# Kernel optimization log

Measured on AMD Instinct MI355X. Metric: run time of the kernel, lower is better.

Reference implementation:

```python
import jax, jax.numpy as jnp
import numpy as np

H = 16          # num_heads
K = 15          # kernel_size (padding_l = K-1, causal)
EPS = 1e-5      # LayerNorm eps


def setup_inputs() -> dict:
    key = jax.random.key(0)
    ks = jax.random.split(key, 8)
    T, B, C, F = 1024, 8, 1024, 4096
    n = lambda k, shape, scale=1.0: jax.random.normal(k, shape, jnp.float32) * scale
    return {
        "x": n(ks[0], (T, B, C)),
        "w_lin": n(ks[1], (C, H * K), 0.02),      # dynamic-conv weight projection
        "b_lin": jnp.zeros((H * K,), jnp.float32),
        "ln_g": jnp.ones((C,), jnp.float32),
        "ln_b": jnp.zeros((C,), jnp.float32),
        "fc1_w": n(ks[2], (C, F), 0.02),
        "fc1_b": jnp.zeros((F,), jnp.float32),
        "fc2_w": n(ks[3], (F, C), 0.02),
        "fc2_b": jnp.zeros((C,), jnp.float32),
    }


def _dynamic_conv(x, w_lin, b_lin):
    # x: (T, B, C). Per-timestep weights -> softmax over kernel -> causal conv.
    T, B, C = x.shape
    R = C // H  # channels per head
    w = jnp.einsum('tbc,ck->tbk', x, w_lin) + b_lin          # (T, B, H*K)
    w = jax.nn.softmax(w.reshape(T, B, H, K), axis=-1)        # softmax over kernel taps
    # causal left-padding: tap k sees x[t + k - (K-1)]
    xp = jnp.pad(x, ((K - 1, 0), (0, 0), (0, 0))).reshape(T + K - 1, B, H, R)
    o = jnp.zeros((T, B, H, R), x.dtype)
    for k in range(K):  # fixed small kernel loop; avoids (T,B,C,K) unfold tensor
        o = o + w[:, :, :, k:k + 1] * xp[k:k + T]
    return o.reshape(T, B, C)


def _layer_norm(y, g, b):
    mu = jnp.mean(y, axis=-1, keepdims=True)
    var = jnp.var(y, axis=-1, keepdims=True)
    return (y - mu) * jax.lax.rsqrt(var + EPS) * g + b


def _forward(x, w_lin, b_lin, ln_g, ln_b, fc1_w, fc1_b, fc2_w, fc2_b):
    y = _dynamic_conv(x, w_lin, b_lin)
    y = _layer_norm(y, ln_g, ln_b)
    h = jax.nn.relu(jnp.einsum('tbc,cf->tbf', y, fc1_w) + fc1_b)
    out = jnp.einsum('tbf,fc->tbc', h, fc2_w) + fc2_b
    return out + y  # residual around FFN (residual taken post-LayerNorm)


def reference(x, w_lin, b_lin, ln_g, ln_b, fc1_w, fc1_b, fc2_w, fc2_b):
    return _forward(x, w_lin, b_lin, ln_g, ln_b, fc1_w, fc1_b, fc2_w, fc2_b)
```

## Files before the change

kernel.cpp:

```cpp
#include <hip/hip_runtime.h>


#define T_DIM 1024
#define B_DIM 8
#define C_DIM 1024
#define F_DIM 4096
#define H_DIM 16
#define K_TAP 15
#define TB (T_DIM * B_DIM)

typedef __attribute__((ext_vector_type(8))) short short8;
typedef __attribute__((ext_vector_type(4))) float f32x4;

__device__ __forceinline__ float bf2f(unsigned short u) {
    union { unsigned int i; float f; } v; v.i = ((unsigned int)u) << 16; return v.f;
}
__device__ __forceinline__ unsigned short f2bf(float f) {
    union { float f; unsigned int i; } v; v.f = f;
    unsigned int r = v.i + 0x7fffu + ((v.i >> 16) & 1u);
    return (unsigned short)(r >> 16);
}

__device__ __forceinline__ void async_copy16(const void* gptr, void* lptr) {
    __builtin_amdgcn_global_load_lds(
        (const __attribute__((address_space(1))) void*)gptr,
        (__attribute__((address_space(3))) void*)lptr, 16, 0, 0);
}

__global__ void cvt_bf16(const float* __restrict__ in, unsigned short* __restrict__ out) {
    int i = (blockIdx.x * 256 + threadIdx.x) * 4;
    float4 v = *(const float4*)(in + i);
    unsigned short a = f2bf(v.x), b = f2bf(v.y), c = f2bf(v.z), d = f2bf(v.w);
    uint2 o;
    o.x = (unsigned int)a | ((unsigned int)b << 16);
    o.y = (unsigned int)c | ((unsigned int)d << 16);
    *(uint2*)(out + i) = o;
}

__global__ void transpose_pad(const float* __restrict__ in,
                              unsigned short* __restrict__ out,
                              int R, int Cin, int Cpad) {
    __shared__ unsigned short tile[32][33];
    const int c0 = blockIdx.x * 32, r0 = blockIdx.y * 32;
    const int x = threadIdx.x, y = threadIdx.y;
#pragma unroll
    for (int j = 0; j < 4; j++) {
        int r = r0 + y + j * 8, c = c0 + x;
        unsigned short v = 0;
        if (c < Cin) v = f2bf(in[(size_t)r * Cin + c]);
        tile[y + j * 8][x] = v;
    }
    __syncthreads();
#pragma unroll
    for (int j = 0; j < 4; j++) {
        out[(size_t)(c0 + y + j * 8) * R + (r0 + x)] = tile[x][y + j * 8];
    }
}

template <int MODE>
__global__ __launch_bounds__(256)
void gemm_bt(const unsigned short* __restrict__ A,
             const unsigned short* __restrict__ Bt,
             void* __restrict__ Cout_v,
             int M, int N, int K,
             const float* __restrict__ bias,
             const unsigned short* __restrict__ resid) {
    __shared__ __align__(16) unsigned short As[2][128 * 32];
    __shared__ __align__(16) unsigned short Bs[2][128 * 32];

    const int tid = threadIdx.x;
    const int m0 = blockIdx.y * 128;
    const int n0 = blockIdx.x * 128;
    const int wave = tid >> 6, lane = tid & 63;
    const int quad = lane >> 4, l16 = lane & 15;
    const int wm = (wave >> 1) * 64;
    const int wn = (wave & 1) * 64;

    f32x4 acc[4][4];
#pragma unroll
    for (int i = 0; i < 4; i++)
#pragma unroll
        for (int j = 0; j < 4; j++) acc[i][j] = (f32x4){0.f, 0.f, 0.f, 0.f};

    const int r_local = lane >> 2;
    const int kc_g = (lane & 3) ^ ((lane >> 3) & 3);
    const unsigned short* gA0 = A + (size_t)(m0 + wave * 32 + r_local) * K + kc_g * 8;
    const unsigned short* gA1 = gA0 + (size_t)16 * K;
    const unsigned short* gB0 = Bt + (size_t)(n0 + wave * 32 + r_local) * K + kc_g * 8;
    const unsigned short* gB1 = gB0 + (size_t)16 * K;
    unsigned short* lA[2] = {&As[0][wave * 32 * 32], &As[1][wave * 32 * 32]};
    unsigned short* lB[2] = {&Bs[0][wave * 32 * 32], &Bs[1][wave * 32 * 32]};

    const int xorsw = (l16 >> 1) & 3;

    async_copy16(gA0, lA[0]);
    async_copy16(gA1, lA[0] + 16 * 32);
    async_copy16(gB0, lB[0]);
    async_copy16(gB1, lB[0] + 16 * 32);

    int buf = 0;
    for (int k0 = 0; k0 < K; k0 += 32) {
        __syncthreads();

        const int nk = k0 + 32;
        if (nk < K) {
            const int nb = buf ^ 1;
            async_copy16(gA0 + nk, lA[nb]);
            async_copy16(gA1 + nk, lA[nb] + 16 * 32);
            async_copy16(gB0 + nk, lB[nb]);
            async_copy16(gB1 + nk, lB[nb] + 16 * 32);
        }

        short8 af[4], bfr[4];
#pragma unroll
        for (int i = 0; i < 4; i++) {
            af[i]  = *(const short8*)(&As[buf][(wm + i * 16 + l16) * 32 + (quad ^ xorsw) * 8]);
            bfr[i] = *(const short8*)(&Bs[buf][(wn + i * 16 + l16) * 32 + (quad ^ xorsw) * 8]);
        }
#pragma unroll
        for (int mi = 0; mi < 4; mi++)
#pragma unroll
            for (int nj = 0; nj < 4; nj++)
                acc[mi][nj] = __builtin_amdgcn_mfma_f32_16x16x32_bf16(
                    af[mi], bfr[nj], acc[mi][nj], 0, 0, 0);
        buf ^= 1;
    }

    const int crow0 = m0 + wm + quad * 4;
    const int ccol0 = n0 + wn + l16;
    if (MODE == 3) {
        float* Cf = (float*)Cout_v;
#pragma unroll
        for (int mi = 0; mi < 4; mi++)
#pragma unroll
            for (int i = 0; i < 4; i++) {
                int rr = crow0 + mi * 16 + i;
#pragma unroll
                for (int nj = 0; nj < 4; nj++)
                    Cf[(size_t)rr * N + ccol0 + nj * 16] = acc[mi][nj][i];
            }
    } else if (MODE == 1) {
        unsigned short* Cb = (unsigned short*)Cout_v;
        float bv[4];
#pragma unroll
        for (int nj = 0; nj < 4; nj++) bv[nj] = bias[ccol0 + nj * 16];
#pragma unroll
        for (int mi = 0; mi < 4; mi++)
#pragma unroll
            for (int i = 0; i < 4; i++) {
                int rr = crow0 + mi * 16 + i;
#pragma unroll
                for (int nj = 0; nj < 4; nj++) {
                    float v = fmaxf(acc[mi][nj][i] + bv[nj], 0.f);
                    Cb[(size_t)rr * N + ccol0 + nj * 16] = f2bf(v);
                }
            }
    } else {
        float* Cf = (float*)Cout_v;
        float bv[4];
#pragma unroll
        for (int nj = 0; nj < 4; nj++) bv[nj] = bias[ccol0 + nj * 16];
#pragma unroll
        for (int mi = 0; mi < 4; mi++)
#pragma unroll
            for (int i = 0; i < 4; i++) {
                int rr = crow0 + mi * 16 + i;
#pragma unroll
                for (int nj = 0; nj < 4; nj++) {
                    float v = acc[mi][nj][i] + bv[nj]
                            + bf2f(resid[(size_t)rr * N + ccol0 + nj * 16]);
                    Cf[(size_t)rr * N + ccol0 + nj * 16] = v;
                }
            }
    }
}

__global__ void softmax_k(const float* __restrict__ wscore,
                          const float* __restrict__ b_lin,
                          float* __restrict__ wconv) {
    int gid = blockIdx.x * 256 + threadIdx.x;
    int row = gid >> 4, hh = gid & 15;
    const float* p = wscore + (size_t)row * 256 + hh * 15;
    float v[K_TAP], mx = -1e30f;
#pragma unroll
    for (int k = 0; k < K_TAP; k++) {
        v[k] = p[k] + b_lin[hh * K_TAP + k];
        mx = fmaxf(mx, v[k]);
    }
    float s = 0.f;
#pragma unroll
    for (int k = 0; k < K_TAP; k++) { v[k] = __expf(v[k] - mx); s += v[k]; }
    float inv = 1.0f / s;
    float* q = wconv + (size_t)row * 240 + hh * K_TAP;
#pragma unroll
    for (int k = 0; k < K_TAP; k++) q[k] = v[k] * inv;
}

__global__ __launch_bounds__(256)
void conv_ln(const unsigned short* __restrict__ x,
             const float* __restrict__ wconv,
             const float* __restrict__ ln_g,
             const float* __restrict__ ln_b,
             unsigned short* __restrict__ y) {
    __shared__ __align__(8) unsigned short xs[K_TAP][C_DIM];
    __shared__ float rbuf[8];
    const int r = blockIdx.x;
    const int t = r >> 3;
    const int tid = threadIdx.x;
    const int c = tid * 4;

#pragma unroll
    for (int k = 0; k < K_TAP; k++) {
        uint2 val = make_uint2(0u, 0u);
        if (t + k >= K_TAP - 1)
            val = *(const uint2*)(x + ((size_t)r + (size_t)(k - (K_TAP - 1)) * B_DIM) * C_DIM + c);
        *(uint2*)(&xs[k][c]) = val;
    }
    __syncthreads();

    const float* wp = wconv + (size_t)r * 240 + (c >> 6) * K_TAP;
    float o0 = 0.f, o1 = 0.f, o2 = 0.f, o3 = 0.f;
#pragma unroll
    for (int k = 0; k < K_TAP; k++) {
        float w = wp[k];
        uint2 xv = *(const uint2*)(&xs[k][c]);
        o0 += w * bf2f((unsigned short)(xv.x & 0xffff));
        o1 += w * bf2f((unsigned short)(xv.x >> 16));
        o2 += w * bf2f((unsigned short)(xv.y & 0xffff));
        o3 += w * bf2f((unsigned short)(xv.y >> 16));
    }
    float s = o0 + o1 + o2 + o3;
    float s2 = o0 * o0 + o1 * o1 + o2 * o2 + o3 * o3;
#pragma unroll
    for (int off = 32; off > 0; off >>= 1) {
        s  += __shfl_down(s, off, 64);
        s2 += __shfl_down(s2, off, 64);
    }
    if ((tid & 63) == 0) { rbuf[tid >> 6] = s; rbuf[(tid >> 6) + 4] = s2; }
    __syncthreads();
    if (tid == 0) {
        rbuf[0] = rbuf[0] + rbuf[1] + rbuf[2] + rbuf[3];
        rbuf[4] = rbuf[4] + rbuf[5] + rbuf[6] + rbuf[7];
    }
    __syncthreads();
    float mu = rbuf[0] * (1.0f / C_DIM);
    float var = rbuf[4] * (1.0f / C_DIM) - mu * mu;
    float rs = rsqrtf(var + 1e-5f);

    float oo[4] = {o0, o1, o2, o3};
    unsigned short o16[4];
#pragma unroll
    for (int j = 0; j < 4; j++)
        o16[j] = f2bf((oo[j] - mu) * rs * ln_g[c + j] + ln_b[c + j]);
    uint2 outv;
    outv.x = (unsigned int)o16[0] | ((unsigned int)o16[1] << 16);
    outv.y = (unsigned int)o16[2] | ((unsigned int)o16[3] << 16);
    *(uint2*)(y + (size_t)r * C_DIM + c) = outv;
}

extern "C" void kernel_launch(void* const* d_in, const int* in_sizes, int n_in,
                              void* d_out, int out_size, void* d_ws, size_t ws_size,
                              hipStream_t stream) {
    const float* x     = (const float*)d_in[0];
    const float* w_lin = (const float*)d_in[1];
    const float* b_lin = (const float*)d_in[2];
    const float* ln_g  = (const float*)d_in[3];
    const float* ln_b  = (const float*)d_in[4];
    const float* fc1_w = (const float*)d_in[5];
    const float* fc1_b = (const float*)d_in[6];
    const float* fc2_w = (const float*)d_in[7];
    const float* fc2_b = (const float*)d_in[8];
    float* out = (float*)d_out;

    char* ws = (char*)d_ws;
    unsigned short* xb    = (unsigned short*)(ws);
    unsigned short* fc1T  = (unsigned short*)(ws + 16777216);
    unsigned short* fc2T  = (unsigned short*)(ws + 25165824);
    unsigned short* wlinT = (unsigned short*)(ws + 33554432);
    unsigned short* y     = (unsigned short*)(ws + 34078720);
    unsigned short* h     = (unsigned short*)(ws + 50855936);
    float* wscore = (float*)(ws + 50855936);
    float* wconv  = (float*)(ws + 59244544);

    cvt_bf16<<<TB * C_DIM / 1024, 256, 0, stream>>>(x, xb);

    dim3 tb(32, 8);
    transpose_pad<<<dim3(F_DIM / 32, C_DIM / 32), tb, 0, stream>>>(fc1_w, fc1T, C_DIM, F_DIM, F_DIM);
    transpose_pad<<<dim3(C_DIM / 32, F_DIM / 32), tb, 0, stream>>>(fc2_w, fc2T, F_DIM, C_DIM, C_DIM);
    transpose_pad<<<dim3(256 / 32, C_DIM / 32), tb, 0, stream>>>(w_lin, wlinT, C_DIM, 240, 256);

    gemm_bt<3><<<dim3(256 / 128, TB / 128), 256, 0, stream>>>(
        xb, wlinT, (void*)wscore, TB, 256, C_DIM, nullptr, nullptr);

    softmax_k<<<TB * H_DIM / 256, 256, 0, stream>>>(wscore, b_lin, wconv);

    conv_ln<<<TB, 256, 0, stream>>>(xb, wconv, ln_g, ln_b, y);

    gemm_bt<1><<<dim3(F_DIM / 128, TB / 128), 256, 0, stream>>>(
        y, fc1T, (void*)h, TB, F_DIM, C_DIM, fc1_b, nullptr);

    gemm_bt<2><<<dim3(C_DIM / 128, TB / 128), 256, 0, stream>>>(
        h, fc2T, (void*)out, TB, C_DIM, F_DIM, fc2_b, y);
}
```

Before: 360.2 us.

## Split-K the weight-projection GEMM and reuse conv windows across eight timesteps

The small C×256 weight-projection GEMM launched only 128 blocks. It now uses a 4-way split-K over blockIdx.z, writing four partial score buffers that the softmax kernel sums. The conv+LayerNorm kernel now has each block handle 8 consecutive timesteps of one batch element. It stages a 22-row x window and the conv weights in LDS, and each wave processes a whole row with 16 channels per lane, so shuffles replace the LDS reduction. The aim is more GPU occupancy for the small GEMM and fewer redundant x loads in the conv, at the cost of extra partial-sum traffic and a larger workspace footprint.

```diff
diff --git a/kernel.cpp b/kernel.cpp
--- a/kernel.cpp
+++ b/kernel.cpp
@@ -62,7 +62,7 @@
 void gemm_bt(const unsigned short* __restrict__ A,
              const unsigned short* __restrict__ Bt,
              void* __restrict__ Cout_v,
-             int M, int N, int K,
+             int M, int N, int K, int kz,
              const float* __restrict__ bias,
              const unsigned short* __restrict__ resid) {
     __shared__ __align__(16) unsigned short As[2][128 * 32];
@@ -71,6 +71,7 @@
     const int tid = threadIdx.x;
     const int m0 = blockIdx.y * 128;
     const int n0 = blockIdx.x * 128;
+    const int kbase = blockIdx.z * kz;
     const int wave = tid >> 6, lane = tid & 63;
     const int quad = lane >> 4, l16 = lane & 15;
     const int wm = (wave >> 1) * 64;
@@ -84,9 +85,9 @@
 
     const int r_local = lane >> 2;
     const int kc_g = (lane & 3) ^ ((lane >> 3) & 3);
-    const unsigned short* gA0 = A + (size_t)(m0 + wave * 32 + r_local) * K + kc_g * 8;
+    const unsigned short* gA0 = A + (size_t)(m0 + wave * 32 + r_local) * K + kbase + kc_g * 8;
     const unsigned short* gA1 = gA0 + (size_t)16 * K;
-    const unsigned short* gB0 = Bt + (size_t)(n0 + wave * 32 + r_local) * K + kc_g * 8;
+    const unsigned short* gB0 = Bt + (size_t)(n0 + wave * 32 + r_local) * K + kbase + kc_g * 8;
     const unsigned short* gB1 = gB0 + (size_t)16 * K;
     unsigned short* lA[2] = {&As[0][wave * 32 * 32], &As[1][wave * 32 * 32]};
     unsigned short* lB[2] = {&Bs[0][wave * 32 * 32], &Bs[1][wave * 32 * 32]};
@@ -99,11 +100,11 @@
     async_copy16(gB1, lB[0] + 16 * 32);
 
     int buf = 0;
-    for (int k0 = 0; k0 < K; k0 += 32) {
+    for (int k0 = 0; k0 < kz; k0 += 32) {
         __syncthreads();
 
         const int nk = k0 + 32;
-        if (nk < K) {
+        if (nk < kz) {
             const int nb = buf ^ 1;
             async_copy16(gA0 + nk, lA[nb]);
             async_copy16(gA1 + nk, lA[nb] + 16 * 32);
@@ -129,7 +130,7 @@
     const int crow0 = m0 + wm + quad * 4;
     const int ccol0 = n0 + wn + l16;
     if (MODE == 3) {
-        float* Cf = (float*)Cout_v;
+        float* Cf = (float*)Cout_v + (size_t)blockIdx.z * M * N;
 #pragma unroll
         for (int mi = 0; mi < 4; mi++)
 #pragma unroll
@@ -175,6 +176,7 @@
     }
 }
 
+#define WS_STRIDE ((size_t)TB * 256)
 __global__ void softmax_k(const float* __restrict__ wscore,
                           const float* __restrict__ b_lin,
                           float* __restrict__ wconv) {
@@ -184,7 +186,8 @@
     float v[K_TAP], mx = -1e30f;
 #pragma unroll
     for (int k = 0; k < K_TAP; k++) {
-        v[k] = p[k] + b_lin[hh * K_TAP + k];
+        v[k] = p[k] + p[k + WS_STRIDE] + p[k + 2 * WS_STRIDE] + p[k + 3 * WS_STRIDE]
+             + b_lin[hh * K_TAP + k];
         mx = fmaxf(mx, v[k]);
     }
     float s = 0.f;
@@ -197,65 +200,82 @@
 }
 
 __global__ __launch_bounds__(256)
-void conv_ln(const unsigned short* __restrict__ x,
-             const float* __restrict__ wconv,
-             const float* __restrict__ ln_g,
-             const float* __restrict__ ln_b,
-             unsigned short* __restrict__ y) {
-    __shared__ __align__(8) unsigned short xs[K_TAP][C_DIM];
-    __shared__ float rbuf[8];
-    const int r = blockIdx.x;
-    const int t = r >> 3;
+void conv_ln8(const unsigned short* __restrict__ x,
+              const float* __restrict__ wconv,
+              const float* __restrict__ ln_g,
+              const float* __restrict__ ln_b,
+              unsigned short* __restrict__ y) {
+    __shared__ __align__(16) unsigned short xs[22][C_DIM];
+    __shared__ float wls[8 * 240];
+    const int blk = blockIdx.x;
+    const int b = blk & 7;
+    const int t0 = (blk >> 3) * 8;
     const int tid = threadIdx.x;
-    const int c = tid * 4;
-
-#pragma unroll
-    for (int k = 0; k < K_TAP; k++) {
+
+#pragma unroll
+    for (int k = 0; k < 22; k++) {
+        int t = t0 + k - 14;
         uint2 val = make_uint2(0u, 0u);
-        if (t + k >= K_TAP - 1)
-            val = *(const uint2*)(x + ((size_t)r + (size_t)(k - (K_TAP - 1)) * B_DIM) * C_DIM + c);
-        *(uint2*)(&xs[k][c]) = val;
+        if (t >= 0)
+            val = *(const uint2*)(x + ((size_t)t * B_DIM + b) * C_DIM + tid * 4);
+        *(uint2*)(&xs[k][tid * 4]) = val;
+    }
+    for (int idx = tid; idx < 8 * 240; idx += 256) {
+        int j = idx / 240, o = idx - j * 240;
+        wls[idx] = wconv[((size_t)(t0 + j) * B_DIM + b) * 240 + o];
     }
     __syncthreads();
 
-    const float* wp = wconv + (size_t)r * 240 + (c >> 6) * K_TAP;
-    float o0 = 0.f, o1 = 0.f, o2 = 0.f, o3 = 0.f;
-#pragma unroll
-    for (int k = 0; k < K_TAP; k++) {
-        float w = wp[k];
-        uint2 xv = *(const uint2*)(&xs[k][c]);
-        o0 += w * bf2f((unsigned short)(xv.x & 0xffff));
-        o1 += w * bf2f((unsigned short)(xv.x >> 16));
-        o2 += w * bf2f((unsigned short)(xv.y & 0xffff));
-        o3 += w * bf2f((unsigned short)(xv.y >> 16));
-    }
-    float s = o0 + o1 + o2 + o3;
-    float s2 = o0 * o0 + o1 * o1 + o2 * o2 + o3 * o3;
-#pragma unroll
-    for (int off = 32; off > 0; off >>= 1) {
-        s  += __shfl_down(s, off, 64);
-        s2 += __shfl_down(s2, off, 64);
-    }
-    if ((tid & 63) == 0) { rbuf[tid >> 6] = s; rbuf[(tid >> 6) + 4] = s2; }
-    __syncthreads();
-    if (tid == 0) {
-        rbuf[0] = rbuf[0] + rbuf[1] + rbuf[2] + rbuf[3];
-        rbuf[4] = rbuf[4] + rbuf[5] + rbuf[6] + rbuf[7];
-    }
-    __syncthreads();
-    float mu = rbuf[0] * (1.0f / C_DIM);
-    float var = rbuf[4] * (1.0f / C_DIM) - mu * mu;
-    float rs = rsqrtf(var + 1e-5f);
-
-    float oo[4] = {o0, o1, o2, o3};
-    unsigned short o16[4];
-#pragma unroll
-    for (int j = 0; j < 4; j++)
-        o16[j] = f2bf((oo[j] - mu) * rs * ln_g[c + j] + ln_b[c + j]);
-    uint2 outv;
-    outv.x = (unsigned int)o16[0] | ((unsigned int)o16[1] << 16);
-    outv.y = (unsigned int)o16[2] | ((unsigned int)o16[3] << 16);
-    *(uint2*)(y + (size_t)r * C_DIM + c) = outv;
+    const int wave = tid >> 6, lane = tid & 63;
+    const int ch0 = lane * 16;
+    const int h = lane >> 2;
+
+    for (int rj = wave; rj < 8; rj += 4) {
+        float acc[16];
+#pragma unroll
+        for (int i = 0; i < 16; i++) acc[i] = 0.f;
+#pragma unroll
+        for (int k = 0; k < K_TAP; k++) {
+            float w = wls[rj * 240 + h * 15 + k];
+            const unsigned short* xr = &xs[rj + k][ch0];
+            uint4 p0 = *(const uint4*)(xr);
+            uint4 p1 = *(const uint4*)(xr + 8);
+            unsigned int uu[8] = {p0.x, p0.y, p0.z, p0.w, p1.x, p1.y, p1.z, p1.w};
+#pragma unroll
+            for (int q = 0; q < 8; q++) {
+                acc[2 * q]     += w * bf2f((unsigned short)(uu[q] & 0xffff));
+                acc[2 * q + 1] += w * bf2f((unsigned short)(uu[q] >> 16));
+            }
+        }
+        float s = 0.f, s2 = 0.f;
+#pragma unroll
+        for (int i = 0; i < 16; i++) { s += acc[i]; s2 += acc[i] * acc[i]; }
+#pragma unroll
+        for (int off = 32; off > 0; off >>= 1) {
+            s  += __shfl_xor(s, off, 64);
+            s2 += __shfl_xor(s2, off, 64);
+        }
+        float mu = s * (1.0f / C_DIM);
+        float var = s2 * (1.0f / C_DIM) - mu * mu;
+        float rs = rsqrtf(var + 1e-5f);
+
+        unsigned short o16[16];
+#pragma unroll
+        for (int i = 0; i < 16; i++)
+            o16[i] = f2bf((acc[i] - mu) * rs * ln_g[ch0 + i] + ln_b[ch0 + i]);
+        uint4 w0, w1;
+        w0.x = (unsigned int)o16[0]  | ((unsigned int)o16[1]  << 16);
+        w0.y = (unsigned int)o16[2]  | ((unsigned int)o16[3]  << 16);
+        w0.z = (unsigned int)o16[4]  | ((unsigned int)o16[5]  << 16);
+        w0.w = (unsigned int)o16[6]  | ((unsigned int)o16[7]  << 16);
+        w1.x = (unsigned int)o16[8]  | ((unsigned int)o16[9]  << 16);
+        w1.y = (unsigned int)o16[10] | ((unsigned int)o16[11] << 16);
+        w1.z = (unsigned int)o16[12] | ((unsigned int)o16[13] << 16);
+        w1.w = (unsigned int)o16[14] | ((unsigned int)o16[15] << 16);
+        unsigned short* yr = y + ((size_t)(t0 + rj) * B_DIM + b) * C_DIM + ch0;
+        *(uint4*)(yr) = w0;
+        *(uint4*)(yr + 8) = w1;
+    }
 }
 
 extern "C" void kernel_launch(void* const* d_in, const int* in_sizes, int n_in,
@@ -280,7 +300,7 @@
     unsigned short* y     = (unsigned short*)(ws + 34078720);
     unsigned short* h     = (unsigned short*)(ws + 50855936);
     float* wscore = (float*)(ws + 50855936);
-    float* wconv  = (float*)(ws + 59244544);
+    float* wconv  = (float*)(ws + 50855936 + 33554432);
 
     cvt_bf16<<<TB * C_DIM / 1024, 256, 0, stream>>>(x, xb);
 
@@ -289,16 +309,16 @@
     transpose_pad<<<dim3(C_DIM / 32, F_DIM / 32), tb, 0, stream>>>(fc2_w, fc2T, F_DIM, C_DIM, C_DIM);
     transpose_pad<<<dim3(256 / 32, C_DIM / 32), tb, 0, stream>>>(w_lin, wlinT, C_DIM, 240, 256);
 
-    gemm_bt<3><<<dim3(256 / 128, TB / 128), 256, 0, stream>>>(
-        xb, wlinT, (void*)wscore, TB, 256, C_DIM, nullptr, nullptr);
+    gemm_bt<3><<<dim3(256 / 128, TB / 128, 4), 256, 0, stream>>>(
+        xb, wlinT, (void*)wscore, TB, 256, C_DIM, C_DIM / 4, nullptr, nullptr);
 
     softmax_k<<<TB * H_DIM / 256, 256, 0, stream>>>(wscore, b_lin, wconv);
 
-    conv_ln<<<TB, 256, 0, stream>>>(xb, wconv, ln_g, ln_b, y);
-
-    gemm_bt<1><<<dim3(F_DIM / 128, TB / 128), 256, 0, stream>>>(
-        y, fc1T, (void*)h, TB, F_DIM, C_DIM, fc1_b, nullptr);
-
-    gemm_bt<2><<<dim3(C_DIM / 128, TB / 128), 256, 0, stream>>>(
-        h, fc2T, (void*)out, TB, C_DIM, F_DIM, fc2_b, y);
-}
+    conv_ln8<<<TB / 8, 256, 0, stream>>>(xb, wconv, ln_g, ln_b, y);
+
+    gemm_bt<1><<<dim3(F_DIM / 128, TB / 128, 1), 256, 0, stream>>>(
+        y, fc1T, (void*)h, TB, F_DIM, C_DIM, C_DIM, fc1_b, nullptr);
+
+    gemm_bt<2><<<dim3(C_DIM / 128, TB / 128, 1), 256, 0, stream>>>(
+        h, fc2T, (void*)out, TB, C_DIM, F_DIM, F_DIM, fc2_b, y);
+}
```

Measured after the change: 356.6 us. No clear change (-1.0%).
